# Kernel optimization log

Hardware: AMD Instinct MI355X
Metric: run time of the kernel (lower is better)

The kernel has to match this reference:

```python
import jax, jax.numpy as jnp
import numpy as np

R, C, N, E, H, F, ED, G, L = 1, 4, 50000, 200000, 128, 128, 16, 64, 2


def setup_inputs() -> dict:
    key = jax.random.key(0)
    ks = jax.random.split(key, 16)
    s = 0.05
    return {
        "x": jax.random.normal(ks[0], (R * C * N, H), jnp.float32),
        "batch": jnp.sort(jax.random.randint(ks[1], (N,), 0, G)),
        "edge_index": jax.random.randint(ks[2], (2, E), 0, N),
        "edge_attr": jax.random.normal(ks[3], (1, 1, E, ED), jnp.float32),
        "node_mask": jax.random.uniform(ks[4], (R, C, N, 1), jnp.float32),
        "edge_mask": jax.random.uniform(ks[5], (R, C, E, 1), jnp.float32),
        "W_be": jax.random.normal(ks[6], (ED, H), jnp.float32) * s,
        "b_be": jnp.zeros((H,), jnp.float32),
        "eps": jnp.zeros((L,), jnp.float32),
        "W1": jax.random.normal(ks[7], (L, H, H), jnp.float32) * s,
        "b1": jnp.zeros((L, H), jnp.float32),
        "W2": jax.random.normal(ks[8], (L, H, H), jnp.float32) * s,
        "b2": jnp.zeros((L, H), jnp.float32),
        "Wm1": jax.random.normal(ks[9], (H, H), jnp.float32) * s,
        "bm1": jnp.zeros((H,), jnp.float32),
        "Wm2": jax.random.normal(ks[10], (H, F), jnp.float32) * s,
        "bm2": jnp.zeros((F,), jnp.float32),
    }


def reference(x, batch, edge_index, edge_attr, node_mask, edge_mask,
              W_be, b_be, eps, W1, b1, W2, b2, Wm1, bm1, Wm2, bm2):
    gelu = lambda v: jax.nn.gelu(v, approximate=False)  # torch F.gelu default is erf
    src, dst = edge_index[0], edge_index[1]
    # bond encoder, shared across conv layers: (1,1,E,H)
    ee = edge_attr @ W_be + b_be
    for l in range(L):
        ux = x.reshape(R, C, N, H)
        # gather + add + GELU + edge-weight multiply: (R,C,E,H)
        msg = gelu(ux[:, :, src, :] + ee) * edge_mask
        # scatter_sum over edges into destination nodes
        agg = jnp.zeros_like(ux).at[:, :, dst, :].add(msg)
        h = (1.0 + eps[l]) * x + agg.reshape(x.shape)
        # conv MLP: Linear -> GELU -> Linear, then outer GELU (norm=Identity, dropout=0)
        h = gelu(h @ W1[l] + b1[l]) @ W2[l] + b2[l]
        x = gelu(h)
    # final node MLP (PyG MLP, norm=None): Linear -> GELU -> Linear
    x = gelu(x @ Wm1 + bm1) @ Wm2 + bm2  # (R*C*N, F)
    x4 = x.reshape(R, C, N, F)
    # masked mean-pool per (repeat, centroid, graph)
    num = jnp.zeros((R, C, G, F), x.dtype).at[:, :, batch, :].add(x4 * node_mask)
    den = jnp.zeros((R, C, G, 1), x.dtype).at[:, :, batch, :].add(node_mask) + 1e-7
    pooled = (num / den).transpose(0, 2, 1, 3).reshape(-1, F)  # (R*G*C, F)
    return pooled
```

## Files before the change

### kernel.cpp

```cpp
#include <hip/hip_runtime.h>
#include <math.h>

#define NN 50000
#define EN 200000
#define CC 4
#define HH 128
#define GG 64
#define LDSA 136
#define LDSF 132

typedef __attribute__((ext_vector_type(8))) short bs8;
typedef __attribute__((ext_vector_type(4))) float f32x4;

__device__ __forceinline__ unsigned short f2bf(float f) {
  unsigned int u = __float_as_uint(f);
  u += 0x7FFFu + ((u >> 16) & 1u);
  return (unsigned short)(u >> 16);
}
__device__ __forceinline__ float bf2f(unsigned short h) {
  return __uint_as_float(((unsigned int)h) << 16);
}
__device__ __forceinline__ float gelu_f(float x) {
  float z = fabsf(x) * 0.7071067811865476f;
  float t = __builtin_amdgcn_rcpf(fmaf(0.3275911f, z, 1.0f));
  float poly = t * fmaf(t, fmaf(t, fmaf(t, fmaf(t, 1.061405429f, -1.453152027f),
                                        1.421413741f), -0.284496736f), 0.254829592f);
  float e = fmaf(-poly, __expf(-z * z), 1.0f);
  return 0.5f * x * (1.0f + copysignf(e, x));
}

__global__ __launch_bounds__(256) void count_kernel(const int* __restrict__ dst,
                                                    int* __restrict__ counts) {
  int e = blockIdx.x * 256 + threadIdx.x;
  if (e < EN) atomicAdd(&counts[dst[e]], 1);
}

__global__ __launch_bounds__(256) void block_sum_kernel(const int* __restrict__ counts,
                                                        int* __restrict__ bsums) {
  int tid = threadIdx.x;
  int i = blockIdx.x * 256 + tid;
  int v = (i < NN) ? counts[i] : 0;
#pragma unroll
  for (int d = 1; d < 64; d <<= 1) v += __shfl_xor(v, d);
  __shared__ int ws4[4];
  if ((tid & 63) == 0) ws4[tid >> 6] = v;
  __syncthreads();
  if (tid == 0) bsums[blockIdx.x] = ws4[0] + ws4[1] + ws4[2] + ws4[3];
}

__global__ __launch_bounds__(256) void bsum_scan_kernel(const int* __restrict__ bsums,
                                                        int* __restrict__ boffs, int nb) {
  int tid = threadIdx.x, lane = tid & 63, wv = tid >> 6;
  int v = (tid < nb) ? bsums[tid] : 0;
  int s = v;
#pragma unroll
  for (int d = 1; d < 64; d <<= 1) { int t = __shfl_up(s, d); if (lane >= d) s += t; }
  __shared__ int wsum[4];
  if (lane == 63) wsum[wv] = s;
  __syncthreads();
  int pre = 0;
  for (int j = 0; j < wv; ++j) pre += wsum[j];
  if (tid < nb) boffs[tid] = pre + s - v;
}

__global__ __launch_bounds__(256) void block_scan_kernel(const int* __restrict__ counts,
                                                         const int* __restrict__ boffs,
                                                         int* __restrict__ offsets,
                                                         int* __restrict__ cursor) {
  int tid = threadIdx.x, lane = tid & 63, wv = tid >> 6;
  int i = blockIdx.x * 256 + tid;
  int v = (i < NN) ? counts[i] : 0;
  int s = v;
#pragma unroll
  for (int d = 1; d < 64; d <<= 1) { int t = __shfl_up(s, d); if (lane >= d) s += t; }
  __shared__ int wsum[4];
  if (lane == 63) wsum[wv] = s;
  __syncthreads();
  int pre = boffs[blockIdx.x];
  for (int j = 0; j < wv; ++j) pre += wsum[j];
  if (i < NN) { int e = pre + s - v; offsets[i] = e; cursor[i] = e; }
  if (i == 0) offsets[NN] = EN;
}

__global__ __launch_bounds__(256) void fill_kernel(const int* __restrict__ dst,
                                                   int* __restrict__ cursor,
                                                   int* __restrict__ csr_e) {
  int e = blockIdx.x * 256 + threadIdx.x;
  if (e < EN) {
    int pos = atomicAdd(&cursor[dst[e]], 1);
    csr_e[pos] = e;
  }
}

__global__ __launch_bounds__(256) void prep_w_kernel(const float* __restrict__ W1,
                                                     const float* __restrict__ W2,
                                                     const float* __restrict__ Wm1,
                                                     const float* __restrict__ Wm2,
                                                     unsigned short* __restrict__ wts) {
  int m = blockIdx.x >> 6;
  int idx = (blockIdx.x & 63) * 256 + threadIdx.x;
  const float* src = (m == 0) ? W1 : (m == 1) ? W1 + 16384 : (m == 2) ? W2
                     : (m == 3) ? W2 + 16384 : (m == 4) ? Wm1 : Wm2;
  unsigned short* dhi = wts + m * 32768;
  unsigned short* dlo = dhi + 16384;
  int n = idx >> 7, k = idx & 127;
  float v = src[k * HH + n];
  unsigned short hi = f2bf(v);
  dhi[n * HH + k] = hi;
  dlo[n * HH + k] = f2bf(v - bf2f(hi));
}

__global__ __launch_bounds__(256) void ee_kernel(const float* __restrict__ eattr,
                                                 const float* __restrict__ Wbe,
                                                 const float* __restrict__ bbe,
                                                 float* __restrict__ ee) {
  __shared__ float Ws[16 * HH];
  __shared__ float Ea[16 * 16];
  int tid = threadIdx.x;
  int e0 = blockIdx.x * 16;
#pragma unroll
  for (int i = 0; i < 8; ++i) Ws[tid + i * 256] = Wbe[tid + i * 256];
  Ea[tid] = eattr[(size_t)e0 * 16 + tid];
  __syncthreads();
  int h = tid & 127, half = tid >> 7;
  float bb = bbe[h];
#pragma unroll
  for (int j = 0; j < 8; ++j) {
    int el = j * 2 + half;
    float acc = bb;
#pragma unroll
    for (int d = 0; d < 16; ++d) acc += Ea[el * 16 + d] * Ws[d * HH + h];
    ee[(size_t)(e0 + el) * HH + h] = acc;
  }
}

__global__ __launch_bounds__(256) void agg_kernel(const float* __restrict__ x,
                                                  const float* __restrict__ ee,
                                                  const float* __restrict__ emask,
                                                  const int* __restrict__ src,
                                                  const int* __restrict__ off,
                                                  const int* __restrict__ csr_e,
                                                  const float* __restrict__ epsp, int layer,
                                                  float* __restrict__ hout) {
  int wv = threadIdx.x >> 6, lane = threadIdx.x & 63;
  int v = blockIdx.x * 4 + wv;
  int half = lane >> 5, l32 = lane & 31;
  int c4 = l32 * 4;
  float4 acc[CC];
#pragma unroll
  for (int c = 0; c < CC; ++c) { acc[c].x = 0.f; acc[c].y = 0.f; acc[c].z = 0.f; acc[c].w = 0.f; }
  int beg = off[v], end = off[v + 1];
  int t0 = beg + half;
  int e = 0, s = 0;
  if (t0 < end) { e = csr_e[t0]; s = src[e]; }
  for (int t = t0; t < end; t += 2) {
    int tn = t + 2;
    int e2 = 0, s2 = 0;
    if (tn < end) { e2 = csr_e[tn]; s2 = src[e2]; }
    float4 ev = *(const float4*)(ee + (size_t)e * HH + c4);
#pragma unroll
    for (int c = 0; c < CC; ++c) {
      float em = emask[c * EN + e];
      float4 xv = *(const float4*)(x + ((size_t)c * NN + s) * HH + c4);
      acc[c].x += gelu_f(xv.x + ev.x) * em;
      acc[c].y += gelu_f(xv.y + ev.y) * em;
      acc[c].z += gelu_f(xv.z + ev.z) * em;
      acc[c].w += gelu_f(xv.w + ev.w) * em;
    }
    e = e2; s = s2;
  }
#pragma unroll
  for (int c = 0; c < CC; ++c) {
    acc[c].x += __shfl_xor(acc[c].x, 32);
    acc[c].y += __shfl_xor(acc[c].y, 32);
    acc[c].z += __shfl_xor(acc[c].z, 32);
    acc[c].w += __shfl_xor(acc[c].w, 32);
  }
  float ep = 1.0f + epsp[layer];
#pragma unroll
  for (int cc = 0; cc < 2; ++cc) {
    int c = half * 2 + cc;
    float4 xs = *(const float4*)(x + ((size_t)c * NN + v) * HH + c4);
    float4 o;
    o.x = fmaf(ep, xs.x, acc[c].x);
    o.y = fmaf(ep, xs.y, acc[c].y);
    o.z = fmaf(ep, xs.z, acc[c].z);
    o.w = fmaf(ep, xs.w, acc[c].w);
    *(float4*)(hout + ((size_t)c * NN + v) * HH + c4) = o;
  }
}

__global__ __launch_bounds__(256, 2) void mlp_kernel(
    const float* __restrict__ in,
    const unsigned short* __restrict__ w1hi, const unsigned short* __restrict__ w1lo,
    const float* __restrict__ b1,
    const unsigned short* __restrict__ w2hi, const unsigned short* __restrict__ w2lo,
    const float* __restrict__ b2,
    float* __restrict__ out) {
  __shared__ __align__(16) unsigned short AB[2 * 64 * HH];
  unsigned short* Ahi = AB;
  unsigned short* Alo = AB + 64 * HH;
  int tid = threadIdx.x;
  int row0 = blockIdx.x * 64;
  int lane = tid & 63, wq = tid >> 6;
  int ln = lane & 15, quad = lane >> 4;

  bs8 b1h[4][2], b1l[4][2];
#pragma unroll
  for (int ks = 0; ks < 4; ++ks)
#pragma unroll
    for (int nt = 0; nt < 2; ++nt) {
      int wrow = ((wq * 2 + nt) * 16 + ln) * HH + ks * 32 + quad * 8;
      b1h[ks][nt] = *(const bs8*)(w1hi + wrow);
      b1l[ks][nt] = *(const bs8*)(w1lo + wrow);
    }

#pragma unroll
  for (int i = 0; i < 4; ++i) {
    int idx = tid + i * 256;
    int r = idx >> 4, blk = idx & 15;
    const float* p = in + (size_t)(row0 + r) * HH + blk * 8;
    float4 v0 = *(const float4*)p;
    float4 v1 = *(const float4*)(p + 4);
    bs8 h, l;
    h[0] = f2bf(v0.x); h[1] = f2bf(v0.y); h[2] = f2bf(v0.z); h[3] = f2bf(v0.w);
    h[4] = f2bf(v1.x); h[5] = f2bf(v1.y); h[6] = f2bf(v1.z); h[7] = f2bf(v1.w);
    l[0] = f2bf(v0.x - bf2f(h[0])); l[1] = f2bf(v0.y - bf2f(h[1]));
    l[2] = f2bf(v0.z - bf2f(h[2])); l[3] = f2bf(v0.w - bf2f(h[3]));
    l[4] = f2bf(v1.x - bf2f(h[4])); l[5] = f2bf(v1.y - bf2f(h[5]));
    l[6] = f2bf(v1.z - bf2f(h[6])); l[7] = f2bf(v1.w - bf2f(h[7]));
    int sb = blk ^ (r & 15);
    *(bs8*)(Ahi + r * HH + sb * 8) = h;
    *(bs8*)(Alo + r * HH + sb * 8) = l;
  }
  __syncthreads();

  f32x4 acc[4][2];
#pragma unroll
  for (int mt = 0; mt < 4; ++mt)
#pragma unroll
    for (int nt = 0; nt < 2; ++nt)
#pragma unroll
      for (int r = 0; r < 4; ++r) acc[mt][nt][r] = 0.f;
#pragma unroll
  for (int ks = 0; ks < 4; ++ks) {
    bs8 ah[4], al[4];
    int sb = ((ks * 4 + quad) ^ ln) * 8;
#pragma unroll
    for (int mt = 0; mt < 4; ++mt) {
      ah[mt] = *(const bs8*)(Ahi + (mt * 16 + ln) * HH + sb);
      al[mt] = *(const bs8*)(Alo + (mt * 16 + ln) * HH + sb);
    }
#pragma unroll
    for (int nt = 0; nt < 2; ++nt)
#pragma unroll
      for (int mt = 0; mt < 4; ++mt) {
        acc[mt][nt] = __builtin_amdgcn_mfma_f32_16x16x32_bf16(al[mt], b1h[ks][nt], acc[mt][nt], 0, 0, 0);
        acc[mt][nt] = __builtin_amdgcn_mfma_f32_16x16x32_bf16(ah[mt], b1l[ks][nt], acc[mt][nt], 0, 0, 0);
        acc[mt][nt] = __builtin_amdgcn_mfma_f32_16x16x32_bf16(ah[mt], b1h[ks][nt], acc[mt][nt], 0, 0, 0);
      }
  }
  __syncthreads();

  bs8 b2h[4][2], b2l[4][2];
#pragma unroll
  for (int ks = 0; ks < 4; ++ks)
#pragma unroll
    for (int nt = 0; nt < 2; ++nt) {
      int wrow = ((wq * 2 + nt) * 16 + ln) * HH + ks * 32 + quad * 8;
      b2h[ks][nt] = *(const bs8*)(w2hi + wrow);
      b2l[ks][nt] = *(const bs8*)(w2lo + wrow);
    }

#pragma unroll
  for (int nt = 0; nt < 2; ++nt) {
    int col = (wq * 2 + nt) * 16 + ln;
    int cb = col >> 3, co = col & 7;
    float bb = b1[col];
#pragma unroll
    for (int mt = 0; mt < 4; ++mt)
#pragma unroll
      for (int r = 0; r < 4; ++r) {
        float tv = gelu_f(acc[mt][nt][r] + bb);
        unsigned short th = f2bf(tv);
        int rr = mt * 16 + quad * 4 + r;
        int sof = rr * HH + (cb ^ (rr & 15)) * 8 + co;
        Ahi[sof] = th;
        Alo[sof] = f2bf(tv - bf2f(th));
      }
  }
  __syncthreads();

#pragma unroll
  for (int mt = 0; mt < 4; ++mt)
#pragma unroll
    for (int nt = 0; nt < 2; ++nt)
#pragma unroll
      for (int r = 0; r < 4; ++r) acc[mt][nt][r] = 0.f;
#pragma unroll
  for (int ks = 0; ks < 4; ++ks) {
    bs8 ah[4], al[4];
    int sb = ((ks * 4 + quad) ^ ln) * 8;
#pragma unroll
    for (int mt = 0; mt < 4; ++mt) {
      ah[mt] = *(const bs8*)(Ahi + (mt * 16 + ln) * HH + sb);
      al[mt] = *(const bs8*)(Alo + (mt * 16 + ln) * HH + sb);
    }
#pragma unroll
    for (int nt = 0; nt < 2; ++nt)
#pragma unroll
      for (int mt = 0; mt < 4; ++mt) {
        acc[mt][nt] = __builtin_amdgcn_mfma_f32_16x16x32_bf16(al[mt], b2h[ks][nt], acc[mt][nt], 0, 0, 0);
        acc[mt][nt] = __builtin_amdgcn_mfma_f32_16x16x32_bf16(ah[mt], b2l[ks][nt], acc[mt][nt], 0, 0, 0);
        acc[mt][nt] = __builtin_amdgcn_mfma_f32_16x16x32_bf16(ah[mt], b2h[ks][nt], acc[mt][nt], 0, 0, 0);
      }
  }
#pragma unroll
  for (int nt = 0; nt < 2; ++nt) {
    int col = (wq * 2 + nt) * 16 + ln;
    float bb = b2[col];
#pragma unroll
    for (int mt = 0; mt < 4; ++mt)
#pragma unroll
      for (int r = 0; r < 4; ++r) {
        float o = gelu_f(acc[mt][nt][r] + bb);
        out[(size_t)(row0 + mt * 16 + quad * 4 + r) * HH + col] = o;
      }
  }
}

__global__ __launch_bounds__(256, 2) void mlp_pool_kernel(
    const float* __restrict__ in,
    const unsigned short* __restrict__ w1hi, const unsigned short* __restrict__ w1lo,
    const float* __restrict__ b1,
    const unsigned short* __restrict__ w2hi, const unsigned short* __restrict__ w2lo,
    const float* __restrict__ b2,
    const float* __restrict__ nmask, const int* __restrict__ batch,
    float* __restrict__ num) {
  __shared__ __align__(16) unsigned short AB[128 * LDSA];
  __shared__ int kk[64];
  unsigned short* Ahi = AB;
  unsigned short* Alo = AB + 64 * LDSA;
  int tid = threadIdx.x;
  int row0 = blockIdx.x * 64;
  int lane = tid & 63, wq = tid >> 6;
  int ln = lane & 15, quad = lane >> 4;

  bs8 b1h[4][2], b1l[4][2];
#pragma unroll
  for (int ks = 0; ks < 4; ++ks)
#pragma unroll
    for (int nt = 0; nt < 2; ++nt) {
      int wrow = ((wq * 2 + nt) * 16 + ln) * HH + ks * 32 + quad * 8;
      b1h[ks][nt] = *(const bs8*)(w1hi + wrow);
      b1l[ks][nt] = *(const bs8*)(w1lo + wrow);
    }
#pragma unroll
  for (int i = 0; i < 8; ++i) {
    int idx = tid + i * 256;
    int r = idx >> 5, cc4 = idx & 31;
    float4 vv = *(const float4*)(in + (size_t)(row0 + r) * HH + cc4 * 4);
    unsigned short h0 = f2bf(vv.x), h1 = f2bf(vv.y), h2 = f2bf(vv.z), h3 = f2bf(vv.w);
    ushort4 hv; hv.x = h0; hv.y = h1; hv.z = h2; hv.w = h3;
    ushort4 lv;
    lv.x = f2bf(vv.x - bf2f(h0)); lv.y = f2bf(vv.y - bf2f(h1));
    lv.z = f2bf(vv.z - bf2f(h2)); lv.w = f2bf(vv.w - bf2f(h3));
    *(ushort4*)(Ahi + r * LDSA + cc4 * 4) = hv;
    *(ushort4*)(Alo + r * LDSA + cc4 * 4) = lv;
  }
  if (tid < 64) {
    int gr = row0 + tid;
    int c = gr / NN;
    int n = gr - c * NN;
    kk[tid] = (c << 6) | batch[n];
  }
  __syncthreads();

  f32x4 acc[4][2];
#pragma unroll
  for (int mt = 0; mt < 4; ++mt)
#pragma unroll
    for (int nt = 0; nt < 2; ++nt)
#pragma unroll
      for (int r = 0; r < 4; ++r) acc[mt][nt][r] = 0.f;
#pragma unroll
  for (int ks = 0; ks < 4; ++ks) {
    bs8 ah[4], al[4];
#pragma unroll
    for (int mt = 0; mt < 4; ++mt) {
      ah[mt] = *(const bs8*)(Ahi + (mt * 16 + ln) * LDSA + ks * 32 + quad * 8);
      al[mt] = *(const bs8*)(Alo + (mt * 16 + ln) * LDSA + ks * 32 + quad * 8);
    }
#pragma unroll
    for (int nt = 0; nt < 2; ++nt)
#pragma unroll
      for (int mt = 0; mt < 4; ++mt) {
        acc[mt][nt] = __builtin_amdgcn_mfma_f32_16x16x32_bf16(al[mt], b1h[ks][nt], acc[mt][nt], 0, 0, 0);
        acc[mt][nt] = __builtin_amdgcn_mfma_f32_16x16x32_bf16(ah[mt], b1l[ks][nt], acc[mt][nt], 0, 0, 0);
        acc[mt][nt] = __builtin_amdgcn_mfma_f32_16x16x32_bf16(ah[mt], b1h[ks][nt], acc[mt][nt], 0, 0, 0);
      }
  }
  __syncthreads();

  bs8 b2h[4][2], b2l[4][2];
#pragma unroll
  for (int ks = 0; ks < 4; ++ks)
#pragma unroll
    for (int nt = 0; nt < 2; ++nt) {
      int wrow = ((wq * 2 + nt) * 16 + ln) * HH + ks * 32 + quad * 8;
      b2h[ks][nt] = *(const bs8*)(w2hi + wrow);
      b2l[ks][nt] = *(const bs8*)(w2lo + wrow);
    }
#pragma unroll
  for (int nt = 0; nt < 2; ++nt) {
    int col = (wq * 2 + nt) * 16 + ln;
    float bb = b1[col];
#pragma unroll
    for (int mt = 0; mt < 4; ++mt)
#pragma unroll
      for (int r = 0; r < 4; ++r) {
        float tv = gelu_f(acc[mt][nt][r] + bb);
        unsigned short th = f2bf(tv);
        int rr = mt * 16 + quad * 4 + r;
        Ahi[rr * LDSA + col] = th;
        Alo[rr * LDSA + col] = f2bf(tv - bf2f(th));
      }
  }
  __syncthreads();

#pragma unroll
  for (int mt = 0; mt < 4; ++mt)
#pragma unroll
    for (int nt = 0; nt < 2; ++nt)
#pragma unroll
      for (int r = 0; r < 4; ++r) acc[mt][nt][r] = 0.f;
#pragma unroll
  for (int ks = 0; ks < 4; ++ks) {
    bs8 ah[4], al[4];
#pragma unroll
    for (int mt = 0; mt < 4; ++mt) {
      ah[mt] = *(const bs8*)(Ahi + (mt * 16 + ln) * LDSA + ks * 32 + quad * 8);
      al[mt] = *(const bs8*)(Alo + (mt * 16 + ln) * LDSA + ks * 32 + quad * 8);
    }
#pragma unroll
    for (int nt = 0; nt < 2; ++nt)
#pragma unroll
      for (int mt = 0; mt < 4; ++mt) {
        acc[mt][nt] = __builtin_amdgcn_mfma_f32_16x16x32_bf16(al[mt], b2h[ks][nt], acc[mt][nt], 0, 0, 0);
        acc[mt][nt] = __builtin_amdgcn_mfma_f32_16x16x32_bf16(ah[mt], b2l[ks][nt], acc[mt][nt], 0, 0, 0);
        acc[mt][nt] = __builtin_amdgcn_mfma_f32_16x16x32_bf16(ah[mt], b2h[ks][nt], acc[mt][nt], 0, 0, 0);
      }
  }
  __syncthreads();
  float* Tf = (float*)AB;
#pragma unroll
  for (int nt = 0; nt < 2; ++nt) {
    int col = (wq * 2 + nt) * 16 + ln;
    float bb = b2[col];
#pragma unroll
    for (int mt = 0; mt < 4; ++mt)
#pragma unroll
      for (int r = 0; r < 4; ++r) {
        int rl = mt * 16 + quad * 4 + r;
        int gr = row0 + rl;
        Tf[rl * LDSF + col] = (acc[mt][nt][r] + bb) * nmask[gr];
      }
  }
  __syncthreads();
  if (tid < 128) {
    int col = tid;
    float a2 = 0.f;
    int cur = kk[0];
    for (int r = 0; r < 64; ++r) {
      int k2 = kk[r];
      if (k2 != cur) {
        atomicAdd(&num[((size_t)(cur & 63) * CC + (cur >> 6)) * HH + col], a2);
        a2 = 0.f;
        cur = k2;
      }
      a2 += Tf[r * LDSF + col];
    }
    atomicAdd(&num[((size_t)(cur & 63) * CC + (cur >> 6)) * HH + col], a2);
  }
}

__global__ __launch_bounds__(256) void pool_finalize_kernel(const float* __restrict__ num,
                                                            const int* __restrict__ batch,
                                                            const float* __restrict__ nmask,
                                                            float* __restrict__ outp) {
  int g = blockIdx.x >> 2, c = blockIdx.x & 3;
  int lo = 0, hi = NN;
  while (lo < hi) { int m = (lo + hi) >> 1; if (batch[m] < g) lo = m + 1; else hi = m; }
  int start = lo;
  hi = NN;
  while (lo < hi) { int m = (lo + hi) >> 1; if (batch[m] < g + 1) lo = m + 1; else hi = m; }
  int end = lo;
  int tid = threadIdx.x;
  float d = 0.f;
  for (int n = start + tid; n < end; n += 256) d += nmask[c * NN + n];
#pragma unroll
  for (int k = 1; k < 64; k <<= 1) d += __shfl_xor(d, k);
  __shared__ float ws4[4];
  if ((tid & 63) == 0) ws4[tid >> 6] = d;
  __syncthreads();
  float den = ws4[0] + ws4[1] + ws4[2] + ws4[3] + 1e-7f;
  if (tid < 128) {
    int idx = blockIdx.x * 128 + tid;
    outp[idx] = num[idx] / den;
  }
}

extern "C" void kernel_launch(void* const* d_in, const int* in_sizes, int n_in,
                              void* d_out, int out_size, void* d_ws, size_t ws_size,
                              hipStream_t stream) {
  const float* x_in  = (const float*)d_in[0];
  const int*   batch = (const int*)d_in[1];
  const int*   eidx  = (const int*)d_in[2];
  const float* eattr = (const float*)d_in[3];
  const float* nmask = (const float*)d_in[4];
  const float* emask = (const float*)d_in[5];
  const float* Wbe   = (const float*)d_in[6];
  const float* bbe   = (const float*)d_in[7];
  const float* epsp  = (const float*)d_in[8];
  const float* W1    = (const float*)d_in[9];
  const float* b1    = (const float*)d_in[10];
  const float* W2    = (const float*)d_in[11];
  const float* b2    = (const float*)d_in[12];
  const float* Wm1   = (const float*)d_in[13];
  const float* bm1   = (const float*)d_in[14];
  const float* Wm2   = (const float*)d_in[15];
  const float* bm2   = (const float*)d_in[16];
  float* outp = (float*)d_out;

  const int* srcp = eidx;
  const int* dstp = eidx + EN;

  char* ws = (char*)d_ws;
  float* ee   = (float*)(ws);
  float* hbuf = (float*)(ws + 102400000);
  float* xbuf = (float*)(ws + 204800000);
  int* counts  = (int*)(ws + 307200000);
  int* offsets = counts + NN;
  int* cursor  = offsets + NN + 1;
  int* csr_e   = cursor + NN;
  unsigned short* wts = (unsigned short*)(ws + 307200000 + 1400016);
  int* bsums = (int*)ws;
  int* boffs = (int*)(ws + 1024);
  float* num = (float*)ws;

  const int NB = (NN + 255) / 256;

  hipMemsetAsync(counts, 0, NN * sizeof(int), stream);
  count_kernel<<<(EN + 255) / 256, 256, 0, stream>>>(dstp, counts);
  block_sum_kernel<<<NB, 256, 0, stream>>>(counts, bsums);
  bsum_scan_kernel<<<1, 256, 0, stream>>>(bsums, boffs, NB);
  block_scan_kernel<<<NB, 256, 0, stream>>>(counts, boffs, offsets, cursor);
  fill_kernel<<<(EN + 255) / 256, 256, 0, stream>>>(dstp, cursor, csr_e);

  prep_w_kernel<<<384, 256, 0, stream>>>(W1, W2, Wm1, Wm2, wts);

  ee_kernel<<<EN / 16, 256, 0, stream>>>(eattr, Wbe, bbe, ee);

  agg_kernel<<<NN / 4, 256, 0, stream>>>(x_in, ee, emask, srcp, offsets, csr_e, epsp, 0, hbuf);
  mlp_kernel<<<(CC * NN) / 64, 256, 0, stream>>>(hbuf, wts + 0, wts + 16384, b1,
                                                 wts + 65536, wts + 81920, b2, xbuf);
  agg_kernel<<<NN / 4, 256, 0, stream>>>(xbuf, ee, emask, srcp, offsets, csr_e, epsp, 1, hbuf);
  mlp_kernel<<<(CC * NN) / 64, 256, 0, stream>>>(hbuf, wts + 32768, wts + 49152, b1 + 128,
                                                 wts + 98304, wts + 114688, b2 + 128, xbuf);
  hipMemsetAsync(num, 0, 131072, stream);
  mlp_pool_kernel<<<(CC * NN) / 64, 256, 0, stream>>>(xbuf, wts + 131072, wts + 147456, bm1,
                                                      wts + 163840, wts + 180224, bm2,
                                                      nmask, batch, num);
  pool_finalize_kernel<<<GG * CC, 256, 0, stream>>>(num, batch, nmask, outp);
}
```

Before: 723.6 us.

## Restructure edge aggregation to one edge per wave with register prefetch

The aggregation kernel stops splitting a node's edges across two half-waves that handle float4 each. Now the full wave processes every edge with float2 per lane, and the next edge's gathered data is software-prefetched into registers. This removes the cross-half shuffle reduction and the half-wave load imbalance on odd edge counts, and the 0.5 GELU factor is folded into the edge mask. In exchange, the loop runs twice as many iterations with narrower loads, and register pressure rises from double-buffering the values for four channels.

New measurement: 714.1 us. About the same (-1.3%).

```diff
diff --git a/kernel.cpp b/kernel.cpp
--- a/kernel.cpp
+++ b/kernel.cpp
@@ -27,6 +27,14 @@
                                         1.421413741f), -0.284496736f), 0.254829592f);
   float e = fmaf(-poly, __expf(-z * z), 1.0f);
   return 0.5f * x * (1.0f + copysignf(e, x));
+}
+__device__ __forceinline__ float gelu2_f(float x) {
+  float z = fabsf(x) * 0.7071067811865476f;
+  float t = __builtin_amdgcn_rcpf(fmaf(0.3275911f, z, 1.0f));
+  float poly = t * fmaf(t, fmaf(t, fmaf(t, fmaf(t, 1.061405429f, -1.453152027f),
+                                        1.421413741f), -0.284496736f), 0.254829592f);
+  float e = fmaf(-poly, __expf(-z * z), 1.0f);
+  return x * (1.0f + copysignf(e, x));
 }
 
 __global__ __launch_bounds__(256) void count_kernel(const int* __restrict__ dst,
@@ -144,49 +152,65 @@
                                                   float* __restrict__ hout) {
   int wv = threadIdx.x >> 6, lane = threadIdx.x & 63;
   int v = blockIdx.x * 4 + wv;
-  int half = lane >> 5, l32 = lane & 31;
-  int c4 = l32 * 4;
-  float4 acc[CC];
-#pragma unroll
-  for (int c = 0; c < CC; ++c) { acc[c].x = 0.f; acc[c].y = 0.f; acc[c].z = 0.f; acc[c].w = 0.f; }
+  int c2 = lane * 2;
+  float2 acc[CC];
+#pragma unroll
+  for (int c = 0; c < CC; ++c) { acc[c].x = 0.f; acc[c].y = 0.f; }
   int beg = off[v], end = off[v + 1];
-  int t0 = beg + half;
-  int e = 0, s = 0;
-  if (t0 < end) { e = csr_e[t0]; s = src[e]; }
-  for (int t = t0; t < end; t += 2) {
-    int tn = t + 2;
-    int e2 = 0, s2 = 0;
-    if (tn < end) { e2 = csr_e[tn]; s2 = src[e2]; }
-    float4 ev = *(const float4*)(ee + (size_t)e * HH + c4);
+
+  float2 eeC; float2 xC[CC]; float emC[CC];
+  int eN = 0, sN = 0;
+  eeC.x = 0.f; eeC.y = 0.f;
+#pragma unroll
+  for (int c = 0; c < CC; ++c) { xC[c].x = 0.f; xC[c].y = 0.f; emC[c] = 0.f; }
+
+  if (beg < end) {
+    int e0 = csr_e[beg];
+    int s0 = src[e0];
+    eeC = *(const float2*)(ee + (size_t)e0 * HH + c2);
 #pragma unroll
     for (int c = 0; c < CC; ++c) {
-      float em = emask[c * EN + e];
-      float4 xv = *(const float4*)(x + ((size_t)c * NN + s) * HH + c4);
-      acc[c].x += gelu_f(xv.x + ev.x) * em;
-      acc[c].y += gelu_f(xv.y + ev.y) * em;
-      acc[c].z += gelu_f(xv.z + ev.z) * em;
-      acc[c].w += gelu_f(xv.w + ev.w) * em;
-    }
-    e = e2; s = s2;
-  }
+      xC[c] = *(const float2*)(x + ((size_t)c * NN + s0) * HH + c2);
+      emC[c] = 0.5f * emask[(size_t)c * EN + e0];
+    }
+    if (beg + 1 < end) { eN = csr_e[beg + 1]; sN = src[eN]; }
+  }
+
+  for (int t = beg; t < end; ++t) {
+    float2 eeB; float2 xB[CC]; float emB[CC];
+    int eNN = 0, sNN = 0;
+    if (t + 1 < end) {
+      eeB = *(const float2*)(ee + (size_t)eN * HH + c2);
+#pragma unroll
+      for (int c = 0; c < CC; ++c) {
+        xB[c] = *(const float2*)(x + ((size_t)c * NN + sN) * HH + c2);
+        emB[c] = 0.5f * emask[(size_t)c * EN + eN];
+      }
+      if (t + 2 < end) { eNN = csr_e[t + 2]; sNN = src[eNN]; }
+    } else {
+      eeB.x = 0.f; eeB.y = 0.f;
+#pragma unroll
+      for (int c = 0; c < CC; ++c) { xB[c].x = 0.f; xB[c].y = 0.f; emB[c] = 0.f; }
+    }
+#pragma unroll
+    for (int c = 0; c < CC; ++c) {
+      acc[c].x += gelu2_f(xC[c].x + eeC.x) * emC[c];
+      acc[c].y += gelu2_f(xC[c].y + eeC.y) * emC[c];
+    }
+    eeC = eeB;
+#pragma unroll
+    for (int c = 0; c < CC; ++c) { xC[c] = xB[c]; emC[c] = emB[c]; }
+    eN = eNN; sN = sNN;
+  }
+
+  float ep = 1.0f + epsp[layer];
 #pragma unroll
   for (int c = 0; c < CC; ++c) {
-    acc[c].x += __shfl_xor(acc[c].x, 32);
-    acc[c].y += __shfl_xor(acc[c].y, 32);
-    acc[c].z += __shfl_xor(acc[c].z, 32);
-    acc[c].w += __shfl_xor(acc[c].w, 32);
-  }
-  float ep = 1.0f + epsp[layer];
-#pragma unroll
-  for (int cc = 0; cc < 2; ++cc) {
-    int c = half * 2 + cc;
-    float4 xs = *(const float4*)(x + ((size_t)c * NN + v) * HH + c4);
-    float4 o;
+    float2 xs = *(const float2*)(x + ((size_t)c * NN + v) * HH + c2);
+    float2 o;
     o.x = fmaf(ep, xs.x, acc[c].x);
     o.y = fmaf(ep, xs.y, acc[c].y);
-    o.z = fmaf(ep, xs.z, acc[c].z);
-    o.w = fmaf(ep, xs.w, acc[c].w);
-    *(float4*)(hout + ((size_t)c * NN + v) * HH + c4) = o;
+    *(float2*)(hout + ((size_t)c * NN + v) * HH + c2) = o;
   }
 }
 
```
